# Optimization experiments

Measured on AMD Instinct MI355X. Metric: run time of the kernel, lower is better.

## Reference

```python
import jax, jax.numpy as jnp
import numpy as np
import math

B, S, D, H, DFF = 16, 512, 1024, 16, 4096
DK = D // H
EPS = 1e-6


def _lin(x, W, b):
    return x @ W + b


def _layernorm(x, g, b):
    # torch-style: unbiased std, eps added to std (not var)
    m = jnp.mean(x, axis=-1, keepdims=True)
    std = jnp.sqrt(jnp.sum((x - m) ** 2, axis=-1, keepdims=True) / (x.shape[-1] - 1))
    return g * (x - m) / (std + EPS) + b


def _gelu(x):
    return 0.5 * x * (1.0 + jnp.tanh(jnp.sqrt(2.0 / jnp.pi) * (x + 0.044715 * x ** 3)))


def setup_inputs() -> dict:
    key = jax.random.key(0)
    ks = jax.random.split(key, 20)
    sc = lambda fan_in: 1.0 / math.sqrt(fan_in)
    d = {
        "x": jax.random.normal(ks[0], (B, S, D), jnp.float32),
        "time": jax.random.normal(ks[1], (B, S, D), jnp.float32),
        "Wq": jax.random.uniform(ks[2], (D, D), jnp.float32, -sc(D), sc(D)),
        "bq": jnp.zeros((D,), jnp.float32),
        "Wk": jax.random.uniform(ks[3], (D, D), jnp.float32, -sc(D), sc(D)),
        "bk": jnp.zeros((D,), jnp.float32),
        "Wt": jax.random.uniform(ks[4], (D, D), jnp.float32, -sc(D), sc(D)),
        "bt": jnp.zeros((D,), jnp.float32),
        "Wv": jax.random.uniform(ks[5], (D, D), jnp.float32, -sc(D), sc(D)),
        "bv": jnp.zeros((D,), jnp.float32),
        "Wo": jax.random.uniform(ks[6], (D, D), jnp.float32, -sc(D), sc(D)),
        "bo": jnp.zeros((D,), jnp.float32),
        "W1": jax.random.uniform(ks[7], (D, DFF), jnp.float32, -sc(D), sc(D)),
        "b1": jnp.zeros((DFF,), jnp.float32),
        "W2": jax.random.uniform(ks[8], (DFF, D), jnp.float32, -sc(DFF), sc(DFF)),
        "b2": jnp.zeros((D,), jnp.float32),
        "ln1_g": jnp.ones((D,), jnp.float32),
        "ln1_b": jnp.zeros((D,), jnp.float32),
        "ln2_g": jnp.ones((D,), jnp.float32),
        "ln2_b": jnp.zeros((D,), jnp.float32),
        "mask_logits": jax.random.uniform(ks[9], (S, S), jnp.float32, 2.0, 5.0),
        "mask": jax.random.randint(ks[10], (B, 1, S, S), 0, 2, jnp.int32),
        "pmask": 0,
    }
    return d


def reference(x, time, Wq, bq, Wk, bk, Wt, bt, Wv, bv, Wo, bo, W1, b1, W2, b2,
              ln1_g, ln1_b, ln2_g, ln2_b, mask_logits, mask, pmask):
    def split_heads(t):  # [B,S,D] -> [B,H,S,DK]
        return t.reshape(B, S, H, DK).transpose(0, 2, 1, 3)

    # --- attention sublayer (dropout = identity at inference) ---
    xn = _layernorm(x, ln1_g, ln1_b)
    q = split_heads(_lin(xn, Wq, bq))
    k1 = split_heads(_lin(xn, Wk, bk))
    k2 = split_heads(_lin(time, Wt, bt))
    v = split_heads(_lin(xn, Wv, bv))

    inv = 1.0 / math.sqrt(DK)
    scores = jnp.einsum("bhqd,bhkd->bhqk", q, k1) * inv
    scores = jnp.where(mask == 0, -1e9, scores)  # masked_fill BEFORE time term
    scores = scores + jnp.einsum("bhqd,bhkd->bhqk", q, k2) * inv
    p_attn = jax.nn.softmax(scores, axis=-1)
    p_attn = p_attn * jax.nn.sigmoid(mask_logits)  # learned post-softmax mask [S,S]
    ctx = jnp.einsum("bhqk,bhkd->bhqd", p_attn, v)
    ctx = ctx.transpose(0, 2, 1, 3).reshape(B, S, D)
    x = x + _lin(ctx, Wo, bo)

    # --- FFN sublayer ---
    xn2 = _layernorm(x, ln2_g, ln2_b)
    ff = _lin(_gelu(_lin(xn2, W1, b1)), W2, b2)
    return x + ff
```

## Files before the change

### kernel.cpp

```cpp
#include <hip/hip_runtime.h>

#define BB   16
#define SS   512
#define DD   1024
#define HH   16
#define DKK  64
#define DFFN 4096
#define LN_EPS 1e-6f
#define QSCALE 0.18033688011112042f

typedef __attribute__((ext_vector_type(8))) __bf16 bf16x8;
typedef __attribute__((ext_vector_type(4))) float f32x4;
typedef __attribute__((ext_vector_type(8))) unsigned short ushort8;
typedef __attribute__((ext_vector_type(4))) unsigned short ushort4_t;

#define AS1 __attribute__((address_space(1)))
#define AS3 __attribute__((address_space(3)))

__device__ __forceinline__ unsigned short f2bf(float f) {
  unsigned int u = __float_as_uint(f);
  u += 0x7FFFu + ((u >> 16) & 1u);
  return (unsigned short)(u >> 16);
}
__device__ __forceinline__ float bf2f(unsigned short u) {
  return __uint_as_float(((unsigned int)u) << 16);
}

__device__ __forceinline__ float gelu_f(float x) {
  float t = 0.7978845608028654f * (x + 0.044715f * x * x * x);
  return x / (1.0f + __expf(-2.0f * t));
}

__device__ __forceinline__ void sbar() {
  __builtin_amdgcn_sched_barrier(0);
  __builtin_amdgcn_s_barrier();
  __builtin_amdgcn_sched_barrier(0);
}
#define WAITVM(N)                                         \
  do {                                                    \
    __builtin_amdgcn_sched_barrier(0);                    \
    asm volatile("s_waitcnt vmcnt(" #N ")" ::: "memory"); \
    __builtin_amdgcn_sched_barrier(0);                    \
  } while (0)

__global__ __launch_bounds__(256) void ln_kernel(const float* __restrict__ x,
                                                 const float* __restrict__ g,
                                                 const float* __restrict__ b,
                                                 unsigned short* __restrict__ out, int ldo) {
  const int row = blockIdx.x;
  const int tid = threadIdx.x;
  const float* xr = x + (size_t)row * DD;
  float4 v = *(const float4*)(xr + tid * 4);
  float s = v.x + v.y + v.z + v.w;
#pragma unroll
  for (int off = 1; off < 64; off <<= 1) s += __shfl_xor(s, off);
  __shared__ float red[8];
  const int wid = tid >> 6, l = tid & 63;
  if (l == 0) red[wid] = s;
  __syncthreads();
  const float mean = (red[0] + red[1] + red[2] + red[3]) * (1.0f / DD);
  float4 d;
  d.x = v.x - mean; d.y = v.y - mean; d.z = v.z - mean; d.w = v.w - mean;
  float ss = d.x * d.x + d.y * d.y + d.z * d.z + d.w * d.w;
#pragma unroll
  for (int off = 1; off < 64; off <<= 1) ss += __shfl_xor(ss, off);
  if (l == 0) red[4 + wid] = ss;
  __syncthreads();
  const float var = (red[4] + red[5] + red[6] + red[7]) * (1.0f / (DD - 1));
  const float scale = 1.0f / (sqrtf(var) + LN_EPS);
  float4 gv = *(const float4*)(g + tid * 4);
  float4 bv = *(const float4*)(b + tid * 4);
  ushort4_t o;
  o[0] = f2bf(gv.x * d.x * scale + bv.x);
  o[1] = f2bf(gv.y * d.y * scale + bv.y);
  o[2] = f2bf(gv.z * d.z * scale + bv.z);
  o[3] = f2bf(gv.w * d.w * scale + bv.w);
  *(ushort4_t*)(out + (size_t)row * ldo + tid * 4) = o;
}

__global__ __launch_bounds__(256) void cvt_bf16(const float* __restrict__ in,
                                                unsigned short* __restrict__ out, int ldo) {
  const int i = blockIdx.x * 256 + threadIdx.x;
  const int row = i >> 7;
  const int c0 = (i & 127) * 8;
  const float4* p = (const float4*)(in + (size_t)row * DD + c0);
  float4 a = p[0], b = p[1];
  ushort8 o;
  o[0] = f2bf(a.x); o[1] = f2bf(a.y); o[2] = f2bf(a.z); o[3] = f2bf(a.w);
  o[4] = f2bf(b.x); o[5] = f2bf(b.y); o[6] = f2bf(b.z); o[7] = f2bf(b.w);
  *(ushort8*)(out + (size_t)row * ldo + c0) = o;
}

__global__ __launch_bounds__(256) void transpose_cvt(const float* __restrict__ W,
                                                     unsigned short* __restrict__ WT,
                                                     int N, int ldo) {
  __shared__ float tile[32][33];
  const int tx = threadIdx.x & 31, ty = threadIdx.x >> 5;
  const int n0 = blockIdx.x * 32, k0 = blockIdx.y * 32;
#pragma unroll
  for (int i = 0; i < 32; i += 8)
    tile[ty + i][tx] = W[(size_t)(k0 + ty + i) * N + n0 + tx];
  __syncthreads();
#pragma unroll
  for (int i = 0; i < 32; i += 8)
    WT[(size_t)(n0 + ty + i) * ldo + k0 + tx] = f2bf(tile[tx][ty + i]);
}

__global__ __launch_bounds__(256) void vtrans(const unsigned short* __restrict__ in,
                                              unsigned short* __restrict__ out) {
  __shared__ unsigned short tile[64][72];
  const int t = threadIdx.x;
  const int c0 = blockIdx.x * 64;
  const int r0 = blockIdx.y * 64;
  const int tx = t & 15, ty = t >> 4;
#pragma unroll
  for (int i = 0; i < 64; i += 16)
    *(ushort4_t*)&tile[ty + i][tx * 4] =
        *(const ushort4_t*)(in + (size_t)(r0 + ty + i) * 1024 + c0 + tx * 4);
  __syncthreads();
  const int cT = t >> 2, rq = (t & 3) * 16;
  ushort8 o0, o1;
#pragma unroll
  for (int j = 0; j < 8; ++j) o0[j] = tile[rq + j][cT];
#pragma unroll
  for (int j = 0; j < 8; ++j) o1[j] = tile[rq + 8 + j][cT];
  *(ushort8*)(out + (size_t)(c0 + cT) * 8192 + r0 + rq) = o0;
  *(ushort8*)(out + (size_t)(c0 + cT) * 8192 + r0 + rq + 8) = o1;
}

__global__ __launch_bounds__(256) void bias_prep(const float* __restrict__ bq,
                                                 const float* __restrict__ bv,
                                                 const float* __restrict__ bk,
                                                 const float* __restrict__ bt,
                                                 float* __restrict__ qvb,
                                                 float* __restrict__ kcb) {
  const int i = blockIdx.x * 256 + threadIdx.x;
  if (i < 2048) qvb[i] = (i < 1024) ? bq[i] : bv[i - 1024];
  else kcb[i - 2048] = bk[i - 2048] + bt[i - 2048];
}

__global__ __launch_bounds__(256) void gate_build(const int* __restrict__ mask,
                                                  const float* __restrict__ ml,
                                                  unsigned short* __restrict__ gate) {
  const int i = blockIdx.x * 256 + threadIdx.x;
  const size_t base = (size_t)i * 8;
  const int off = (int)(base & (SS * SS - 1));
  const int4* mp = (const int4*)(mask + base);
  const int4 m0 = mp[0], m1 = mp[1];
  const float4* lp = (const float4*)(ml + off);
  const float4 a = lp[0], b = lp[1];
  ushort8 o;
  o[0] = m0.x ? f2bf(1.0f / (1.0f + __expf(-a.x))) : 0;
  o[1] = m0.y ? f2bf(1.0f / (1.0f + __expf(-a.y))) : 0;
  o[2] = m0.z ? f2bf(1.0f / (1.0f + __expf(-a.z))) : 0;
  o[3] = m0.w ? f2bf(1.0f / (1.0f + __expf(-a.w))) : 0;
  o[4] = m1.x ? f2bf(1.0f / (1.0f + __expf(-b.x))) : 0;
  o[5] = m1.y ? f2bf(1.0f / (1.0f + __expf(-b.y))) : 0;
  o[6] = m1.z ? f2bf(1.0f / (1.0f + __expf(-b.z))) : 0;
  o[7] = m1.w ? f2bf(1.0f / (1.0f + __expf(-b.w))) : 0;
  *(ushort8*)(gate + base) = o;
}

template <int BM, int EPI>
__global__ __launch_bounds__(512, 2) void gemm8p(const unsigned short* __restrict__ A, int lda,
                                                 const unsigned short* __restrict__ BT,
                                                 const float* __restrict__ bias,
                                                 const float* __restrict__ resid,
                                                 void* __restrict__ Cout,
                                                 unsigned short* __restrict__ vOut,
                                                 int M, int N, int K) {
  constexpr int MI = BM / 32;
  constexpr int ASUB = BM / 16;
  constexpr int AHALF = BM * 32;
  constexpr int ABUF = BM * 64;
  constexpr int ACALL = BM / 128;

  __shared__ __align__(16) unsigned short smA[2 * ABUF];
  __shared__ __align__(16) unsigned short smB[2 * 16384];

  const int tid = threadIdx.x;
  const int w = tid >> 6, lane = tid & 63;
  const int lr = lane & 15, lg = lane >> 4;
  const int wr = w >> 2, wn = w & 3;

  const int nb = N / 256;
  const int nwg = gridDim.x;
  int bid = blockIdx.x;
  bid = (bid & 7) * (nwg >> 3) + (bid >> 3);
  const int mb = bid / nb, nbk = bid % nb;

  const int uo = (lane * 16) ^ (lane & 32);
  const int srow = uo >> 6;
  const int scol = (uo & 63) >> 1;

  const unsigned short* pA[2];
  const unsigned short* pB[2];
#pragma unroll
  for (int j = 0; j < ACALL; ++j)
    pA[j] = A + (size_t)(mb * BM + (j * 8 + w) * 16 + srow) * lda + scol;
  if (ACALL == 1) pA[1] = pA[0];
#pragma unroll
  for (int j = 0; j < 2; ++j)
    pB[j] = BT + (size_t)(nbk * 256 + (j * 8 + w) * 16 + srow) * K + scol;

  auto stA = [&](int kt, int ks, int j, int d) {
    __builtin_amdgcn_global_load_lds(
        (const AS1 void*)(pA[j] + (size_t)kt * 64 + ks * 32),
        (AS3 void*)(smA + d * ABUF + ks * AHALF + j * 4096 + w * 512), 16, 0, 0);
  };
  auto stB = [&](int kt, int ks, int j, int d) {
    __builtin_amdgcn_global_load_lds(
        (const AS1 void*)(pB[j] + (size_t)kt * 64 + ks * 32),
        (AS3 void*)(smB + d * 16384 + ks * 8192 + j * 4096 + w * 512), 16, 0, 0);
  };
  auto issue_half = [&](int t, int ks) {
    const int d = t & 1;
#pragma unroll
    for (int j = 0; j < ACALL; ++j) stA(t, ks, j, d);
    stB(t, ks, 0, d);
    stB(t, ks, 1, d);
  };

  const int aoff = lr * 32 + ((lg * 8) ^ ((lr & 8) << 1));

  f32x4 acc[MI][4] = {};
  const int NT = K >> 6;

  issue_half(0, 0);
  issue_half(0, 1);
  issue_half(1, 0);
  if constexpr (ACALL == 2) { WAITVM(8); } else { WAITVM(6); }
  sbar();

  for (int kt = 0; kt < NT; ++kt) {
    const unsigned short* aD = smA + (kt & 1) * ABUF;
    const unsigned short* bD = smB + (kt & 1) * 16384;
    const bool i1 = (kt + 1 < NT);
    const bool i2 = (kt + 2 < NT);
    bf16x8 af[4], bf[4];

#pragma unroll
    for (int i = 0; i < 4; ++i)
      bf[i] = *(const bf16x8*)(bD + (wn * 4 + i) * 512 + aoff);
#pragma unroll
    for (int i = 0; i < 4; ++i)
      af[i] = *(const bf16x8*)(aD + (wr * MI + i) * 512 + aoff);
    if (i1) issue_half(kt + 1, 1);
    if constexpr (ACALL == 1) {
      if (i1) { WAITVM(6); } else { WAITVM(0); }
    }
    sbar();
    __builtin_amdgcn_s_setprio(1);
#pragma unroll
    for (int mi = 0; mi < 4; ++mi)
#pragma unroll
      for (int ni = 0; ni < 4; ++ni)
        acc[mi][ni] = __builtin_amdgcn_mfma_f32_16x16x32_bf16(af[mi], bf[ni], acc[mi][ni], 0, 0, 0);
    __builtin_amdgcn_s_setprio(0);
    sbar();

    if constexpr (ACALL == 2) {
#pragma unroll
      for (int i = 0; i < 4; ++i)
        af[i] = *(const bf16x8*)(aD + (wr * MI + 4 + i) * 512 + aoff);
      if (i1) { WAITVM(8); } else { WAITVM(0); }
      sbar();
      __builtin_amdgcn_s_setprio(1);
#pragma unroll
      for (int mi = 0; mi < 4; ++mi)
#pragma unroll
        for (int ni = 0; ni < 4; ++ni)
          acc[4 + mi][ni] = __builtin_amdgcn_mfma_f32_16x16x32_bf16(af[mi], bf[ni], acc[4 + mi][ni], 0, 0, 0);
      __builtin_amdgcn_s_setprio(0);
      sbar();
    }

#pragma unroll
    for (int i = 0; i < 4; ++i)
      bf[i] = *(const bf16x8*)(bD + (16 + wn * 4 + i) * 512 + aoff);
#pragma unroll
    for (int i = 0; i < 4; ++i)
      af[i] = *(const bf16x8*)(aD + (ASUB + wr * MI + i) * 512 + aoff);
    if (i2) issue_half(kt + 2, 0);
    if constexpr (ACALL == 1) {
      if (i2) { WAITVM(6); } else { WAITVM(3); }
    }
    sbar();
    __builtin_amdgcn_s_setprio(1);
#pragma unroll
    for (int mi = 0; mi < 4; ++mi)
#pragma unroll
      for (int ni = 0; ni < 4; ++ni)
        acc[mi][ni] = __builtin_amdgcn_mfma_f32_16x16x32_bf16(af[mi], bf[ni], acc[mi][ni], 0, 0, 0);
    __builtin_amdgcn_s_setprio(0);
    sbar();

    if constexpr (ACALL == 2) {
#pragma unroll
      for (int i = 0; i < 4; ++i)
        af[i] = *(const bf16x8*)(aD + (ASUB + wr * MI + 4 + i) * 512 + aoff);
      if (i2) { WAITVM(8); } else { WAITVM(4); }
      sbar();
      __builtin_amdgcn_s_setprio(1);
#pragma unroll
      for (int mi = 0; mi < 4; ++mi)
#pragma unroll
        for (int ni = 0; ni < 4; ++ni)
          acc[4 + mi][ni] = __builtin_amdgcn_mfma_f32_16x16x32_bf16(af[mi], bf[ni], acc[4 + mi][ni], 0, 0, 0);
      __builtin_amdgcn_s_setprio(0);
      sbar();
    }
  }

  const int colb = nbk * 256 + wn * 64;
  const int rowb = mb * BM + wr * (BM / 2);
  float bvv[4];
#pragma unroll
  for (int ni = 0; ni < 4; ++ni) bvv[ni] = bias[colb + ni * 16 + lr];

  if (EPI == 3 && colb >= 1024) {
#pragma unroll
    for (int mi = 0; mi < MI; ++mi) {
#pragma unroll
      for (int j = 0; j < 4; ++j) {
        const int row = rowb + mi * 16 + lg * 4 + j;
#pragma unroll
        for (int ni = 0; ni < 4; ++ni)
          vOut[(size_t)row * 1024 + (colb - 1024) + ni * 16 + lr] = f2bf(acc[mi][ni][j] + bvv[ni]);
      }
    }
  } else {
#pragma unroll
    for (int mi = 0; mi < MI; ++mi) {
#pragma unroll
      for (int j = 0; j < 4; ++j) {
        const int row = rowb + mi * 16 + lg * 4 + j;
#pragma unroll
        for (int ni = 0; ni < 4; ++ni) {
          const int col = colb + ni * 16 + lr;
          float vv = acc[mi][ni][j] + bvv[ni];
          if (EPI == 2) vv = gelu_f(vv);
          if (EPI == 1) {
            const size_t o = (size_t)row * N + col;
            ((float*)Cout)[o] = vv + resid[o];
          } else if (EPI == 3) {
            ((unsigned short*)Cout)[(size_t)row * 1024 + col] = f2bf(vv * QSCALE);
          } else {
            ((unsigned short*)Cout)[(size_t)row * N + col] = f2bf(vv);
          }
        }
      }
    }
  }
}

template <int EPI>
__global__ __launch_bounds__(256, 2) void gemm128(const unsigned short* __restrict__ A, int lda,
                                                  const unsigned short* __restrict__ BT,
                                                  const float* __restrict__ bias,
                                                  const float* __restrict__ resid,
                                                  void* __restrict__ Cout,
                                                  int M, int N, int K) {
  __shared__ __align__(16) unsigned short smA[2 * 8192];
  __shared__ __align__(16) unsigned short smB[2 * 8192];

  const int tid = threadIdx.x;
  const int w = tid >> 6, lane = tid & 63;
  const int lr = lane & 15, lg = lane >> 4;
  const int wr = w >> 1, wn = w & 1;

  const int nb = N / 128;
  const int nwg = gridDim.x;
  int bid = blockIdx.x;
  bid = (bid & 7) * (nwg >> 3) + (bid >> 3);
  const int mb = bid / nb, nbk = bid % nb;

  const int uo = (lane * 16) ^ (lane & 32);
  const int srow = uo >> 6;
  const int scol = (uo & 63) >> 1;

  const unsigned short* pA[2];
  const unsigned short* pB[2];
#pragma unroll
  for (int j = 0; j < 2; ++j) {
    pA[j] = A + (size_t)(mb * 128 + (j * 4 + w) * 16 + srow) * lda + scol;
    pB[j] = BT + (size_t)(nbk * 128 + (j * 4 + w) * 16 + srow) * K + scol;
  }

  auto stA = [&](int kt, int ks, int j, int d) {
    __builtin_amdgcn_global_load_lds(
        (const AS1 void*)(pA[j] + (size_t)kt * 64 + ks * 32),
        (AS3 void*)(smA + d * 8192 + ks * 4096 + j * 2048 + w * 512), 16, 0, 0);
  };
  auto stB = [&](int kt, int ks, int j, int d) {
    __builtin_amdgcn_global_load_lds(
        (const AS1 void*)(pB[j] + (size_t)kt * 64 + ks * 32),
        (AS3 void*)(smB + d * 8192 + ks * 4096 + j * 2048 + w * 512), 16, 0, 0);
  };
  auto issue_half = [&](int t, int ks) {
    const int d = t & 1;
    stA(t, ks, 0, d); stA(t, ks, 1, d);
    stB(t, ks, 0, d); stB(t, ks, 1, d);
  };

  const int aoff = lr * 32 + ((lg * 8) ^ ((lr & 8) << 1));

  f32x4 acc[4][4] = {};
  const int NT = K >> 6;

  issue_half(0, 0);
  issue_half(0, 1);
  issue_half(1, 0);
  WAITVM(8);
  sbar();

  for (int kt = 0; kt < NT; ++kt) {
    const unsigned short* aD = smA + (kt & 1) * 8192;
    const unsigned short* bD = smB + (kt & 1) * 8192;
    const bool i1 = (kt + 1 < NT);
    const bool i2 = (kt + 2 < NT);
    bf16x8 af[4], bf[4];

#pragma unroll
    for (int i = 0; i < 4; ++i)
      bf[i] = *(const bf16x8*)(bD + (wn * 4 + i) * 512 + aoff);
#pragma unroll
    for (int i = 0; i < 4; ++i)
      af[i] = *(const bf16x8*)(aD + (wr * 4 + i) * 512 + aoff);
    if (i1) issue_half(kt + 1, 1);
    if (i1) { WAITVM(8); } else { WAITVM(0); }
    sbar();
    __builtin_amdgcn_s_setprio(1);
#pragma unroll
    for (int mi = 0; mi < 4; ++mi)
#pragma unroll
      for (int ni = 0; ni < 4; ++ni)
        acc[mi][ni] = __builtin_amdgcn_mfma_f32_16x16x32_bf16(af[mi], bf[ni], acc[mi][ni], 0, 0, 0);
    __builtin_amdgcn_s_setprio(0);
    sbar();

#pragma unroll
    for (int i = 0; i < 4; ++i)
      bf[i] = *(const bf16x8*)(bD + 4096 + (wn * 4 + i) * 512 + aoff);
#pragma unroll
    for (int i = 0; i < 4; ++i)
      af[i] = *(const bf16x8*)(aD + 4096 + (wr * 4 + i) * 512 + aoff);
    if (i2) issue_half(kt + 2, 0);
    if (i2) { WAITVM(8); } else if (i1) { WAITVM(4); } else { WAITVM(0); }
    sbar();
    __builtin_amdgcn_s_setprio(1);
#pragma unroll
    for (int mi = 0; mi < 4; ++mi)
#pragma unroll
      for (int ni = 0; ni < 4; ++ni)
        acc[mi][ni] = __builtin_amdgcn_mfma_f32_16x16x32_bf16(af[mi], bf[ni], acc[mi][ni], 0, 0, 0);
    __builtin_amdgcn_s_setprio(0);
    sbar();
  }

  const int colb = nbk * 128 + wn * 64;
  const int rowb = mb * 128 + wr * 64;
  float bvv[4];
#pragma unroll
  for (int ni = 0; ni < 4; ++ni) bvv[ni] = bias[colb + ni * 16 + lr];
#pragma unroll
  for (int mi = 0; mi < 4; ++mi) {
#pragma unroll
    for (int j = 0; j < 4; ++j) {
      const int row = rowb + mi * 16 + lg * 4 + j;
#pragma unroll
      for (int ni = 0; ni < 4; ++ni) {
        const int col = colb + ni * 16 + lr;
        const float vv = acc[mi][ni][j] + bvv[ni];
        if (EPI == 1) {
          const size_t o = (size_t)row * N + col;
          ((float*)Cout)[o] = vv + resid[o];
        } else {
          ((unsigned short*)Cout)[(size_t)row * N + col] = f2bf(vv);
        }
      }
    }
  }
}

__global__ __launch_bounds__(256) void attn4(const unsigned short* __restrict__ qb,
                                             const unsigned short* __restrict__ vT,
                                             const unsigned short* __restrict__ kcb,
                                             const unsigned short* __restrict__ gate,
                                             unsigned short* __restrict__ ctx) {
  __shared__ __align__(16) unsigned char smem[33280];
  float* pctx = (float*)smem;
  float* sumw = (float*)(smem + 32768);

  const int tid = threadIdx.x;
  const int w = tid >> 6, l = tid & 63;
  const int lr = l & 15, lg = l >> 4;
  const int virt = (blockIdx.x & 7) * 512 + (blockIdx.x >> 3);
  const int qt = virt & 15;
  const int h = (virt >> 4) & 15;
  const int b = virt >> 8;
  const int q0 = qt * 32;

  const unsigned short* qg = qb + (size_t)b * SS * DD + h * DKK;
  const unsigned short* kg = kcb + (size_t)b * SS * DD + h * DKK;
  const unsigned short* vg = vT + (size_t)(h * DKK) * 8192 + b * SS;
  const unsigned short* gg = gate + (size_t)b * SS * SS;
  unsigned short* cg = ctx + (size_t)b * SS * DD + h * DKK;

  bf16x8 qf[2][2];
#pragma unroll
  for (int mi = 0; mi < 2; ++mi)
#pragma unroll
    for (int ks = 0; ks < 2; ++ks)
      qf[mi][ks] = *(const bf16x8*)(qg + (size_t)(q0 + mi * 16 + lr) * DD + ks * 32 + lg * 8);

  f32x4 acc[2][4] = {};
  float ssum[2][4] = {};
  const int kb0 = w * 128;

#pragma unroll
  for (int it = 0; it < 4; ++it) {
    const int kbase = kb0 + it * 32;
    unsigned short* Pb = (unsigned short*)smem + w * 2560 + (it & 1) * 1280;

    bf16x8 kf[2][2];
#pragma unroll
    for (int ni = 0; ni < 2; ++ni)
#pragma unroll
      for (int ks = 0; ks < 2; ++ks)
        kf[ni][ks] = *(const bf16x8*)(kg + (size_t)(kbase + ni * 16 + lr) * DD + ks * 32 + lg * 8);
    f32x4 sc[2][2] = {};
#pragma unroll
    for (int ks = 0; ks < 2; ++ks)
#pragma unroll
      for (int mi = 0; mi < 2; ++mi)
#pragma unroll
        for (int ni = 0; ni < 2; ++ni)
          sc[mi][ni] = __builtin_amdgcn_mfma_f32_16x16x32_bf16(qf[mi][ks], kf[ni][ks], sc[mi][ni], 0, 0, 0);

    bf16x8 vb[4];
#pragma unroll
    for (int dkg = 0; dkg < 4; ++dkg)
      vb[dkg] = *(const bf16x8*)(vg + (size_t)(dkg * 16 + lr) * 8192 + kbase + lg * 8);

#pragma unroll
    for (int mi = 0; mi < 2; ++mi)
#pragma unroll
      for (int ni = 0; ni < 2; ++ni)
#pragma unroll
        for (int j = 0; j < 4; ++j) {
          const int row = mi * 16 + lg * 4 + j;
          const unsigned short gu = gg[(size_t)(q0 + row) * SS + kbase + ni * 16 + lr];
          const float e = exp2f(sc[mi][ni][j]);
          ssum[mi][j] += gu ? e : 0.0f;
          Pb[row * 40 + ni * 16 + lr] = f2bf(e * bf2f(gu));
        }

#pragma unroll
    for (int mi = 0; mi < 2; ++mi) {
      const bf16x8 pa = *(const bf16x8*)(Pb + (mi * 16 + lr) * 40 + lg * 8);
#pragma unroll
      for (int dkg = 0; dkg < 4; ++dkg)
        acc[mi][dkg] = __builtin_amdgcn_mfma_f32_16x16x32_bf16(pa, vb[dkg], acc[mi][dkg], 0, 0, 0);
    }
  }

#pragma unroll
  for (int mi = 0; mi < 2; ++mi)
#pragma unroll
    for (int j = 0; j < 4; ++j) {
      float s = ssum[mi][j];
      s += __shfl_xor(s, 1);
      s += __shfl_xor(s, 2);
      s += __shfl_xor(s, 4);
      s += __shfl_xor(s, 8);
      if (lr == 0) sumw[w * 32 + mi * 16 + lg * 4 + j] = s;
    }
  __syncthreads();

#pragma unroll
  for (int mi = 0; mi < 2; ++mi)
#pragma unroll
    for (int dkg = 0; dkg < 4; ++dkg)
#pragma unroll
      for (int j = 0; j < 4; ++j)
        pctx[(size_t)w * 2048 + (mi * 16 + lg * 4 + j) * 64 + dkg * 16 + lr] = acc[mi][dkg][j];
  __syncthreads();

  {
    const int row = tid >> 3;
    const int dk0 = (tid & 7) * 8;
    const float tot = sumw[row] + sumw[32 + row] + sumw[64 + row] + sumw[96 + row];
    const float inv = 1.0f / fmaxf(tot, 1e-30f);
    float vsum[8];
#pragma unroll
    for (int c = 0; c < 8; ++c) vsum[c] = 0.0f;
#pragma unroll
    for (int ww = 0; ww < 4; ++ww) {
      const float* p = pctx + (size_t)ww * 2048 + row * 64 + dk0;
      f32x4 a = *(const f32x4*)p;
      f32x4 bq = *(const f32x4*)(p + 4);
#pragma unroll
      for (int c = 0; c < 4; ++c) { vsum[c] += a[c]; vsum[4 + c] += bq[c]; }
    }
    ushort8 o;
#pragma unroll
    for (int c = 0; c < 8; ++c) o[c] = f2bf(vsum[c] * inv);
    *(ushort8*)(cg + (size_t)(q0 + row) * DD + dk0) = o;
  }
}

extern "C" void kernel_launch(void* const* d_in, const int* in_sizes, int n_in,
                              void* d_out, int out_size, void* d_ws, size_t ws_size,
                              hipStream_t stream) {
  (void)in_sizes; (void)n_in; (void)out_size; (void)ws_size;
  const float* x    = (const float*)d_in[0];
  const float* timep= (const float*)d_in[1];
  const float* Wq = (const float*)d_in[2];  const float* bq = (const float*)d_in[3];
  const float* Wk = (const float*)d_in[4];  const float* bk = (const float*)d_in[5];
  const float* Wt = (const float*)d_in[6];  const float* bt = (const float*)d_in[7];
  const float* Wv = (const float*)d_in[8];  const float* bv = (const float*)d_in[9];
  const float* Wo = (const float*)d_in[10]; const float* bo = (const float*)d_in[11];
  const float* W1 = (const float*)d_in[12]; const float* b1 = (const float*)d_in[13];
  const float* W2 = (const float*)d_in[14]; const float* b2 = (const float*)d_in[15];
  const float* ln1g = (const float*)d_in[16]; const float* ln1b = (const float*)d_in[17];
  const float* ln2g = (const float*)d_in[18]; const float* ln2b = (const float*)d_in[19];
  const float* ml   = (const float*)d_in[20];
  const int*   mask = (const int*)d_in[21];
  float* out = (float*)d_out;

  char* w = (char*)d_ws;
  auto alloc = [&](size_t sz) { char* p = w; w += (sz + 255) & ~(size_t)255; return p; };
  const int MT = BB * SS;

  unsigned short* WqvT = (unsigned short*)alloc((size_t)2048 * 1024 * 2);
  unsigned short* WkcT = (unsigned short*)alloc((size_t)1024 * 2048 * 2);
  unsigned short* WoT  = (unsigned short*)alloc((size_t)DD * DD * 2);
  unsigned short* W1T  = (unsigned short*)alloc((size_t)DD * DFFN * 2);
  unsigned short* W2T  = (unsigned short*)alloc((size_t)DFFN * DD * 2);
  float* qvb = (float*)alloc(2048 * 4);
  float* kcbias = (float*)alloc(1024 * 4);
  unsigned short* gateb = (unsigned short*)alloc((size_t)BB * SS * SS * 2);
  unsigned short* xt2 = (unsigned short*)alloc((size_t)MT * 2048 * 2);
  unsigned short* qbuf = (unsigned short*)alloc((size_t)MT * DD * 2);
  unsigned short* vbuf = (unsigned short*)alloc((size_t)MT * DD * 2);
  unsigned short* vTb = (unsigned short*)alloc((size_t)DD * MT * 2);
  unsigned short* kcb = (unsigned short*)alloc((size_t)MT * DD * 2);
  float*          x2  = (float*)alloc((size_t)MT * DD * 4);
  unsigned short* hb  = (unsigned short*)alloc((size_t)MT * DFFN * 2);
  unsigned short* ctx = xt2;
  unsigned short* xn2 = xt2;

  transpose_cvt<<<dim3(32, 32), 256, 0, stream>>>(Wq, WqvT, 1024, 1024);
  transpose_cvt<<<dim3(32, 32), 256, 0, stream>>>(Wv, WqvT + (size_t)1024 * 1024, 1024, 1024);
  transpose_cvt<<<dim3(32, 32), 256, 0, stream>>>(Wk, WkcT, 1024, 2048);
  transpose_cvt<<<dim3(32, 32), 256, 0, stream>>>(Wt, WkcT + 1024, 1024, 2048);
  transpose_cvt<<<dim3(32, 32), 256, 0, stream>>>(Wo, WoT, 1024, 1024);
  transpose_cvt<<<dim3(128, 32), 256, 0, stream>>>(W1, W1T, 4096, 1024);
  transpose_cvt<<<dim3(32, 128), 256, 0, stream>>>(W2, W2T, 1024, 4096);
  bias_prep<<<dim3(12), 256, 0, stream>>>(bq, bv, bk, bt, qvb, kcbias);
  gate_build<<<dim3(BB * SS * SS / 8 / 256), 256, 0, stream>>>(mask, ml, gateb);

  ln_kernel<<<dim3(MT), 256, 0, stream>>>(x, ln1g, ln1b, xt2, 2048);
  cvt_bf16<<<dim3(MT * DD / 8 / 256), 256, 0, stream>>>(timep, xt2 + 1024, 2048);

  gemm8p<256, 3><<<dim3(256), 512, 0, stream>>>(xt2, 2048, WqvT, qvb, nullptr, (void*)qbuf, vbuf, MT, 2048, 1024);
  vtrans<<<dim3(16, 128), 256, 0, stream>>>(vbuf, vTb);
  gemm128<0><<<dim3(512), 256, 0, stream>>>(xt2, 2048, WkcT, kcbias, nullptr, (void*)kcb, MT, 1024, 2048);

  attn4<<<dim3(BB * HH * 16), 256, 0, stream>>>(qbuf, vTb, kcb, gateb, ctx);

  gemm128<1><<<dim3(512), 256, 0, stream>>>(ctx, 1024, WoT, bo, x, (void*)x2, MT, 1024, 1024);
  ln_kernel<<<dim3(MT), 256, 0, stream>>>(x2, ln2g, ln2b, xn2, 1024);
  gemm8p<256, 2><<<dim3(512), 512, 0, stream>>>(xn2, 1024, W1T, b1, nullptr, (void*)hb, nullptr, MT, 4096, 1024);
  gemm128<1><<<dim3(512), 256, 0, stream>>>(hb, 4096, W2T, b2, x2, (void*)out, MT, 1024, 4096);
}
```

Measured before the change: 448.0 us.

## Repartition attention so each wave owns 16 query rows over all keys

The attention kernel used to split the key range across four waves, each covering 32 query rows, and then merge the partial contexts and row sums through shared memory with two block barriers. Now each block has two waves, each wave owns 16 query rows and loops over all 512 keys. The row sums are reduced inside the wave and the context is written straight to global memory. This removes the 33KB cross-wave reduction buffer and the barriers, cuts register use, and allows more blocks per CU. In exchange each K and V tile is loaded by two waves instead of being shared across a 32-row tile, and each wave runs a longer serial loop.

```diff
diff --git a/kernel.cpp b/kernel.cpp
--- a/kernel.cpp
+++ b/kernel.cpp
@@ -483,14 +483,12 @@
   }
 }
 
-__global__ __launch_bounds__(256) void attn4(const unsigned short* __restrict__ qb,
-                                             const unsigned short* __restrict__ vT,
-                                             const unsigned short* __restrict__ kcb,
-                                             const unsigned short* __restrict__ gate,
-                                             unsigned short* __restrict__ ctx) {
-  __shared__ __align__(16) unsigned char smem[33280];
-  float* pctx = (float*)smem;
-  float* sumw = (float*)(smem + 32768);
+__global__ __launch_bounds__(128, 4) void attn5(const unsigned short* __restrict__ qb,
+                                                const unsigned short* __restrict__ vT,
+                                                const unsigned short* __restrict__ kcb,
+                                                const unsigned short* __restrict__ gate,
+                                                unsigned short* __restrict__ ctx) {
+  __shared__ __align__(16) unsigned short Pl[2][2][16 * 40];
 
   const int tid = threadIdx.x;
   const int w = tid >> 6, l = tid & 63;
@@ -499,115 +497,77 @@
   const int qt = virt & 15;
   const int h = (virt >> 4) & 15;
   const int b = virt >> 8;
-  const int q0 = qt * 32;
+  const int q0 = qt * 32 + w * 16;
 
   const unsigned short* qg = qb + (size_t)b * SS * DD + h * DKK;
-  const unsigned short* kg = kcb + (size_t)b * SS * DD + h * DKK;
-  const unsigned short* vg = vT + (size_t)(h * DKK) * 8192 + b * SS;
-  const unsigned short* gg = gate + (size_t)b * SS * SS;
+  const unsigned short* kg = kcb + (size_t)b * SS * DD + h * DKK + (size_t)lr * DD + lg * 8;
+  const unsigned short* vg = vT + (size_t)(h * DKK + lr) * 8192 + b * SS + lg * 8;
+  const unsigned short* gg = gate + (size_t)b * SS * SS + (size_t)(q0 + lg * 4) * SS + lr;
   unsigned short* cg = ctx + (size_t)b * SS * DD + h * DKK;
 
-  bf16x8 qf[2][2];
-#pragma unroll
-  for (int mi = 0; mi < 2; ++mi)
+  bf16x8 qf[2];
+#pragma unroll
+  for (int ks = 0; ks < 2; ++ks)
+    qf[ks] = *(const bf16x8*)(qg + (size_t)(q0 + lr) * DD + ks * 32 + lg * 8);
+
+  f32x4 acc[4] = {};
+  float ssum[4] = {};
+
+#pragma unroll 4
+  for (int kt = 0; kt < 16; ++kt) {
+    const int kbase = kt * 32;
+    unsigned short* Pb = Pl[w][kt & 1];
+
+    bf16x8 kf[2][2];
+#pragma unroll
+    for (int ni = 0; ni < 2; ++ni)
+#pragma unroll
+      for (int ks = 0; ks < 2; ++ks)
+        kf[ni][ks] = *(const bf16x8*)(kg + (size_t)(kbase + ni * 16) * DD + ks * 32);
+    f32x4 sc[2] = {};
 #pragma unroll
     for (int ks = 0; ks < 2; ++ks)
-      qf[mi][ks] = *(const bf16x8*)(qg + (size_t)(q0 + mi * 16 + lr) * DD + ks * 32 + lg * 8);
-
-  f32x4 acc[2][4] = {};
-  float ssum[2][4] = {};
-  const int kb0 = w * 128;
-
-#pragma unroll
-  for (int it = 0; it < 4; ++it) {
-    const int kbase = kb0 + it * 32;
-    unsigned short* Pb = (unsigned short*)smem + w * 2560 + (it & 1) * 1280;
-
-    bf16x8 kf[2][2];
+#pragma unroll
+      for (int ni = 0; ni < 2; ++ni)
+        sc[ni] = __builtin_amdgcn_mfma_f32_16x16x32_bf16(qf[ks], kf[ni][ks], sc[ni], 0, 0, 0);
+
+    bf16x8 vb[4];
+#pragma unroll
+    for (int dkg = 0; dkg < 4; ++dkg)
+      vb[dkg] = *(const bf16x8*)(vg + (size_t)(dkg * 16) * 8192 + kbase);
+
+    const unsigned short* gp = gg + kbase;
 #pragma unroll
     for (int ni = 0; ni < 2; ++ni)
 #pragma unroll
-      for (int ks = 0; ks < 2; ++ks)
-        kf[ni][ks] = *(const bf16x8*)(kg + (size_t)(kbase + ni * 16 + lr) * DD + ks * 32 + lg * 8);
-    f32x4 sc[2][2] = {};
-#pragma unroll
-    for (int ks = 0; ks < 2; ++ks)
-#pragma unroll
-      for (int mi = 0; mi < 2; ++mi)
-#pragma unroll
-        for (int ni = 0; ni < 2; ++ni)
-          sc[mi][ni] = __builtin_amdgcn_mfma_f32_16x16x32_bf16(qf[mi][ks], kf[ni][ks], sc[mi][ni], 0, 0, 0);
-
-    bf16x8 vb[4];
+      for (int j = 0; j < 4; ++j) {
+        const unsigned short gu = gp[(size_t)j * SS + ni * 16];
+        const float e = exp2f(sc[ni][j]);
+        ssum[j] += gu ? e : 0.0f;
+        Pb[(lg * 4 + j) * 40 + ni * 16 + lr] = f2bf(e * bf2f(gu));
+      }
+
+    const bf16x8 pa = *(const bf16x8*)(Pb + lr * 40 + lg * 8);
 #pragma unroll
     for (int dkg = 0; dkg < 4; ++dkg)
-      vb[dkg] = *(const bf16x8*)(vg + (size_t)(dkg * 16 + lr) * 8192 + kbase + lg * 8);
-
-#pragma unroll
-    for (int mi = 0; mi < 2; ++mi)
-#pragma unroll
-      for (int ni = 0; ni < 2; ++ni)
-#pragma unroll
-        for (int j = 0; j < 4; ++j) {
-          const int row = mi * 16 + lg * 4 + j;
-          const unsigned short gu = gg[(size_t)(q0 + row) * SS + kbase + ni * 16 + lr];
-          const float e = exp2f(sc[mi][ni][j]);
-          ssum[mi][j] += gu ? e : 0.0f;
-          Pb[row * 40 + ni * 16 + lr] = f2bf(e * bf2f(gu));
-        }
-
-#pragma unroll
-    for (int mi = 0; mi < 2; ++mi) {
-      const bf16x8 pa = *(const bf16x8*)(Pb + (mi * 16 + lr) * 40 + lg * 8);
-#pragma unroll
-      for (int dkg = 0; dkg < 4; ++dkg)
-        acc[mi][dkg] = __builtin_amdgcn_mfma_f32_16x16x32_bf16(pa, vb[dkg], acc[mi][dkg], 0, 0, 0);
-    }
+      acc[dkg] = __builtin_amdgcn_mfma_f32_16x16x32_bf16(pa, vb[dkg], acc[dkg], 0, 0, 0);
   }
 
-#pragma unroll
-  for (int mi = 0; mi < 2; ++mi)
-#pragma unroll
-    for (int j = 0; j < 4; ++j) {
-      float s = ssum[mi][j];
-      s += __shfl_xor(s, 1);
-      s += __shfl_xor(s, 2);
-      s += __shfl_xor(s, 4);
-      s += __shfl_xor(s, 8);
-      if (lr == 0) sumw[w * 32 + mi * 16 + lg * 4 + j] = s;
-    }
-  __syncthreads();
-
-#pragma unroll
-  for (int mi = 0; mi < 2; ++mi)
-#pragma unroll
-    for (int dkg = 0; dkg < 4; ++dkg)
-#pragma unroll
-      for (int j = 0; j < 4; ++j)
-        pctx[(size_t)w * 2048 + (mi * 16 + lg * 4 + j) * 64 + dkg * 16 + lr] = acc[mi][dkg][j];
-  __syncthreads();
-
-  {
-    const int row = tid >> 3;
-    const int dk0 = (tid & 7) * 8;
-    const float tot = sumw[row] + sumw[32 + row] + sumw[64 + row] + sumw[96 + row];
-    const float inv = 1.0f / fmaxf(tot, 1e-30f);
-    float vsum[8];
-#pragma unroll
-    for (int c = 0; c < 8; ++c) vsum[c] = 0.0f;
-#pragma unroll
-    for (int ww = 0; ww < 4; ++ww) {
-      const float* p = pctx + (size_t)ww * 2048 + row * 64 + dk0;
-      f32x4 a = *(const f32x4*)p;
-      f32x4 bq = *(const f32x4*)(p + 4);
-#pragma unroll
-      for (int c = 0; c < 4; ++c) { vsum[c] += a[c]; vsum[4 + c] += bq[c]; }
-    }
-    ushort8 o;
-#pragma unroll
-    for (int c = 0; c < 8; ++c) o[c] = f2bf(vsum[c] * inv);
-    *(ushort8*)(cg + (size_t)(q0 + row) * DD + dk0) = o;
+  float inv[4];
+#pragma unroll
+  for (int j = 0; j < 4; ++j) {
+    float s = ssum[j];
+    s += __shfl_xor(s, 1);
+    s += __shfl_xor(s, 2);
+    s += __shfl_xor(s, 4);
+    s += __shfl_xor(s, 8);
+    inv[j] = 1.0f / fmaxf(s, 1e-30f);
   }
+#pragma unroll
+  for (int dkg = 0; dkg < 4; ++dkg)
+#pragma unroll
+    for (int j = 0; j < 4; ++j)
+      cg[(size_t)(q0 + lg * 4 + j) * DD + dkg * 16 + lr] = f2bf(acc[dkg][j] * inv[j]);
 }
 
 extern "C" void kernel_launch(void* const* d_in, const int* in_sizes, int n_in,
@@ -668,7 +628,7 @@
   vtrans<<<dim3(16, 128), 256, 0, stream>>>(vbuf, vTb);
   gemm128<0><<<dim3(512), 256, 0, stream>>>(xt2, 2048, WkcT, kcbias, nullptr, (void*)kcb, MT, 1024, 2048);
 
-  attn4<<<dim3(BB * HH * 16), 256, 0, stream>>>(qbuf, vTb, kcb, gateb, ctx);
+  attn5<<<dim3(BB * HH * 16), 128, 0, stream>>>(qbuf, vTb, kcb, gateb, ctx);
 
   gemm128<1><<<dim3(512), 256, 0, stream>>>(ctx, 1024, WoT, bo, x, (void*)x2, MT, 1024, 1024);
   ln_kernel<<<dim3(MT), 256, 0, stream>>>(x2, ln2g, ln2b, xn2, 1024);
```

Measured after the change: 499.6 us. +11.5%, slower.
